# Kernel optimization log

Measured on AMD Instinct MI355X. Metric: run time of the kernel, lower is better.

## Reference

```python
import jax, jax.numpy as jnp
import numpy as np

EPS = 1e-5

def _ln(x, gamma, beta):
    mu = jnp.mean(x, axis=-1, keepdims=True)
    var = jnp.mean(jnp.square(x - mu), axis=-1, keepdims=True)
    return (x - mu) * jax.lax.rsqrt(var + EPS) * gamma + beta

def _linear(x, w, b):
    # torch nn.Linear convention: w is [out, in]
    return jnp.einsum('...i,oi->...o', x, w) + b

def setup_inputs() -> dict:
    key = jax.random.key(0)
    B, L, C = 1, 384, 128
    ks = jax.random.split(key, 16)
    s = 1.0 / np.sqrt(C)
    inp = {
        'pair_feat': jax.random.normal(ks[0], (B, L, L, C), dtype=jnp.float32),
        'res_mask': jnp.ones((B, L), dtype=jnp.float32),
        # left_proj: Linear + LayerNorm
        'lp_w': jax.random.uniform(ks[1], (C, C), jnp.float32, -s, s),
        'lp_b': jnp.zeros((C,), jnp.float32),
        'lp_g': jnp.ones((C,), jnp.float32),
        'lp_beta': jnp.zeros((C,), jnp.float32),
        # right_proj: Linear + LayerNorm
        'rp_w': jax.random.uniform(ks[2], (C, C), jnp.float32, -s, s),
        'rp_b': jnp.zeros((C,), jnp.float32),
        'rp_g': jnp.ones((C,), jnp.float32),
        'rp_beta': jnp.zeros((C,), jnp.float32),
        # gates: Linear (then sigmoid)
        'lg_w': jax.random.uniform(ks[3], (C, C), jnp.float32, -s, s),
        'lg_b': jnp.zeros((C,), jnp.float32),
        'rg_w': jax.random.uniform(ks[4], (C, C), jnp.float32, -s, s),
        'rg_b': jnp.zeros((C,), jnp.float32),
        'og_w': jax.random.uniform(ks[5], (C, C), jnp.float32, -s, s),
        'og_b': jnp.zeros((C,), jnp.float32),
        # out_layer: LayerNorm + Linear
        'ol_g': jnp.ones((C,), jnp.float32),
        'ol_beta': jnp.zeros((C,), jnp.float32),
        'ow': jax.random.uniform(ks[6], (C, C), jnp.float32, -s, s),
        'ob': jnp.zeros((C,), jnp.float32),
    }
    return inp

def reference(pair_feat, res_mask, lp_w, lp_b, lp_g, lp_beta,
              rp_w, rp_b, rp_g, rp_beta, lg_w, lg_b, rg_w, rg_b,
              og_w, og_b, ol_g, ol_beta, ow, ob):
    # op_type == 'outgoing': einsum 'bikc,bjkc->bijc'
    proj_left = _ln(_linear(pair_feat, lp_w, lp_b), lp_g, lp_beta)
    proj_right = _ln(_linear(pair_feat, rp_w, rp_b), rp_g, rp_beta)
    mask2d = (res_mask[:, :, None] * res_mask[:, None, :])[..., None]  # [B,L,L,1]
    proj_left = proj_left * mask2d
    proj_right = proj_right * mask2d
    gate_left = jax.nn.sigmoid(_linear(pair_feat, lg_w, lg_b))
    gate_right = jax.nn.sigmoid(_linear(pair_feat, rg_w, rg_b))
    proj_left = proj_left * gate_left
    proj_right = proj_right * gate_right
    out = jnp.einsum('bikc,bjkc->bijc', proj_left, proj_right)
    out = _linear(_ln(out, ol_g, ol_beta), ow, ob)
    gate = jax.nn.sigmoid(_linear(pair_feat, og_w, og_b))
    return out * gate
```

## Files before the change

### kernel.cpp

```cpp
#include <hip/hip_runtime.h>

typedef __bf16 bf16x8 __attribute__((ext_vector_type(8)));
typedef __bf16 bf16x4 __attribute__((ext_vector_type(4)));
typedef float  f32x4  __attribute__((ext_vector_type(4)));
typedef int    int4v  __attribute__((ext_vector_type(4)));

#define LL    384
#define CC    128
#define NROW  (LL * LL)

#define MFMA16(a, b, c) __builtin_amdgcn_mfma_f32_16x16x32_bf16((a), (b), (c), 0, 0, 0)

__device__ __forceinline__ bf16x8 cvt8(const float* p) {
    f32x4 a = *reinterpret_cast<const f32x4*>(p);
    f32x4 b = *reinterpret_cast<const f32x4*>(p + 4);
    bf16x8 r;
    r[0] = (__bf16)a[0]; r[1] = (__bf16)a[1]; r[2] = (__bf16)a[2]; r[3] = (__bf16)a[3];
    r[4] = (__bf16)b[0]; r[5] = (__bf16)b[1]; r[6] = (__bf16)b[2]; r[7] = (__bf16)b[3];
    return r;
}
__device__ __forceinline__ bf16x8 ld_ws(const __bf16* p) {
    return __builtin_bit_cast(bf16x8, *reinterpret_cast<const int4v*>(p));
}
__device__ __forceinline__ float sigmf(float x) { return 1.f / (1.f + __expf(-x)); }

__device__ __forceinline__ void gl16(const __bf16* g, __bf16* l) {
    __builtin_amdgcn_global_load_lds(
        (const __attribute__((address_space(1))) unsigned int*)g,
        (__attribute__((address_space(3))) unsigned int*)l,
        16, 0, 0);
}

__device__ __forceinline__ void stage_weight(const float* __restrict__ w,
                                             __bf16* dst, int tid) {
    const int c   = tid >> 1;
    const int k0  = (tid & 1) * 64;
    const int nt  = c >> 4;
    const int n16 = c & 15;
    #pragma unroll
    for (int u = 0; u < 8; ++u) {
        const int k    = k0 + u * 8;
        const int ks   = k >> 5;
        const int quad = (k >> 3) & 3;
        bf16x8 v = cvt8(w + c * CC + k);
        *reinterpret_cast<int4v*>(dst + ((ks * 8 + nt) * 64 + quad * 16 + n16) * 8) =
            __builtin_bit_cast(int4v, v);
    }
}
__device__ __forceinline__ bf16x8 wfrag(const __bf16* base, int ks, int nt, int lane) {
    return ld_ws(base + ((ks * 8 + nt) * 64 + lane) * 8);
}

__global__ __launch_bounds__(256) void k_wconv(
    const float* __restrict__ w0, const float* __restrict__ w1,
    const float* __restrict__ w2, const float* __restrict__ w3,
    const float* __restrict__ w4, const float* __restrict__ w5,
    __bf16* __restrict__ dst)
{
    const float* srcs[6] = {w0, w1, w2, w3, w4, w5};
    stage_weight(srcs[blockIdx.x], dst + (size_t)blockIdx.x * 16384, threadIdx.x);
}

__global__ __launch_bounds__(256, 2) void k_proj(
    const float* __restrict__ pf, const float* __restrict__ rmask,
    const __bf16* __restrict__ wfm,
    const float* __restrict__ lp_b, const float* __restrict__ lp_g,
    const float* __restrict__ lp_be,
    const float* __restrict__ rp_b, const float* __restrict__ rp_g,
    const float* __restrict__ rp_be,
    const float* __restrict__ lg_b, const float* __restrict__ rg_b,
    __bf16* __restrict__ pl_c, __bf16* __restrict__ pr_c)
{
    __shared__ __bf16 wl[2][16384];

    const int tid  = threadIdx.x;
    const int wave = tid >> 6, lane = tid & 63;
    const int n16  = lane & 15, quad = lane >> 4;
    const int rowblock = blockIdx.x * 128 + wave * 32;

    auto STAGEW = [&](int widx, __bf16* dstL) {
        const __bf16* src = wfm + (size_t)widx * 16384;
        #pragma unroll
        for (int i = 0; i < 8; ++i) {
            const int s = wave * 8 + i;
            gl16(src + (size_t)s * 512 + lane * 8, dstL + (size_t)s * 512);
        }
    };

    bf16x8 xf[2][4];
    #pragma unroll
    for (int rg = 0; rg < 2; ++rg) {
        const int r_a = rowblock + rg * 16 + n16;
        #pragma unroll
        for (int ks = 0; ks < 4; ++ks)
            xf[rg][ks] = cvt8(pf + (size_t)r_a * CC + ks * 32 + quad * 8);
    }

    float mrow[2][4];
    #pragma unroll
    for (int rg = 0; rg < 2; ++rg) {
        const int rd   = rowblock + rg * 16 + quad * 4;
        const int i_id = rd / LL;
        const int k_id = rd - i_id * LL;
        float mi = rmask[i_id];
        #pragma unroll
        for (int g = 0; g < 4; ++g) mrow[rg][g] = mi * rmask[k_id + g];
    }

    f32x4 acc[2][8];
    auto GEMM = [&](const __bf16* wb) {
        #pragma unroll
        for (int rg = 0; rg < 2; ++rg)
            #pragma unroll
            for (int nt = 0; nt < 8; ++nt) acc[rg][nt] = f32x4{0.f, 0.f, 0.f, 0.f};
        #pragma unroll
        for (int ks = 0; ks < 4; ++ks)
            #pragma unroll
            for (int nt = 0; nt < 8; ++nt) {
                bf16x8 wf = wfrag(wb, ks, nt, lane);
                #pragma unroll
                for (int rg = 0; rg < 2; ++rg)
                    acc[rg][nt] = MFMA16(xf[rg][ks], wf, acc[rg][nt]);
            }
    };

    bf16x4 sg[2][8];
    auto SIGM = [&](const float* gb) {
        #pragma unroll
        for (int rg = 0; rg < 2; ++rg)
            #pragma unroll
            for (int nt = 0; nt < 8; ++nt) {
                float bias = gb[nt * 16 + n16];
                #pragma unroll
                for (int g = 0; g < 4; ++g)
                    sg[rg][nt][g] = (__bf16)sigmf(acc[rg][nt][g] + bias);
            }
    };

    auto EPILOG = [&](const float* pb, const float* gamma, const float* beta,
                      __bf16* dst) {
        #pragma unroll
        for (int rg = 0; rg < 2; ++rg) {
            #pragma unroll
            for (int nt = 0; nt < 8; ++nt) {
                float bias = pb[nt * 16 + n16];
                #pragma unroll
                for (int g = 0; g < 4; ++g) acc[rg][nt][g] += bias;
            }
            float s[4] = {0.f,0.f,0.f,0.f}, ss[4] = {0.f,0.f,0.f,0.f};
            #pragma unroll
            for (int nt = 0; nt < 8; ++nt)
                #pragma unroll
                for (int g = 0; g < 4; ++g) { float v = acc[rg][nt][g]; s[g] += v; ss[g] += v * v; }
            #pragma unroll
            for (int m = 1; m < 16; m <<= 1)
                #pragma unroll
                for (int g = 0; g < 4; ++g) {
                    s[g]  += __shfl_xor(s[g],  m, 64);
                    ss[g] += __shfl_xor(ss[g], m, 64);
                }
            float mean[4], rstd[4];
            #pragma unroll
            for (int g = 0; g < 4; ++g) {
                mean[g] = s[g] * (1.f / 128.f);
                float var = ss[g] * (1.f / 128.f) - mean[g] * mean[g];
                rstd[g] = rsqrtf(fmaxf(var, 0.f) + 1e-5f);
            }
            const int rd = rowblock + rg * 16 + quad * 4;
            #pragma unroll
            for (int nt = 0; nt < 8; ++nt) {
                const int c = nt * 16 + n16;
                float ga = gamma[c], be = beta[c];
                bf16x4 o;
                #pragma unroll
                for (int g = 0; g < 4; ++g) {
                    float v = (acc[rg][nt][g] - mean[g]) * rstd[g] * ga + be;
                    v *= mrow[rg][g] * (float)sg[rg][nt][g];
                    o[g] = (__bf16)v;
                }
                *reinterpret_cast<bf16x4*>(dst + (size_t)c * NROW + rd) = o;
            }
        }
    };

    STAGEW(0, wl[0]);
    __syncthreads();

    STAGEW(1, wl[1]);
    GEMM(wl[0]);  SIGM(lg_b);
    __syncthreads();

    STAGEW(2, wl[0]);
    GEMM(wl[1]);  EPILOG(lp_b, lp_g, lp_be, pl_c);
    __syncthreads();

    STAGEW(3, wl[1]);
    GEMM(wl[0]);  SIGM(rg_b);
    __syncthreads();

    GEMM(wl[1]);  EPILOG(rp_b, rp_g, rp_be, pr_c);
}

__global__ __launch_bounds__(256, 3) void k_einsum_tile(
    const __bf16* __restrict__ pl_c, const __bf16* __restrict__ pr_c,
    float* __restrict__ T)
{
    __shared__ __bf16 sA[2][512 * 8];
    __shared__ __bf16 sB[2][512 * 8];

    const int bid  = blockIdx.x;
    const int wgid = (bid & 7) * 144 + (bid >> 3);
    const int ch   = wgid / 9;
    const int tile = wgid - ch * 9;
    const int i0   = (tile / 3) * 128;
    const int j0   = (tile % 3) * 128;

    const int tid  = threadIdx.x;
    const int w    = tid >> 6, lane = tid & 63;
    const int n16  = lane & 15, quad = lane >> 4;
    const int wr   = w >> 1, wc = w & 1;

    const __bf16* Pc = pl_c + (size_t)ch * NROW;
    const __bf16* Qc = pr_c + (size_t)ch * NROW;

    const __bf16* ga[2];
    const __bf16* gb[2];
    #pragma unroll
    for (int u = 0; u < 2; ++u) {
        const int row = (w * 2 + u) * 16 + n16;
        ga[u] = Pc + (size_t)(i0 + row) * LL + quad * 8;
        gb[u] = Qc + (size_t)(j0 + row) * LL + quad * 8;
    }

    f32x4 acc[4][4];
    #pragma unroll
    for (int m = 0; m < 4; ++m)
        #pragma unroll
        for (int n = 0; n < 4; ++n) acc[m][n] = f32x4{0.f, 0.f, 0.f, 0.f};

    auto STAGE = [&](int buf, int k0) {
        #pragma unroll
        for (int u = 0; u < 2; ++u) {
            __bf16* la = &sA[buf][(size_t)((w * 2 + u) * 64) * 8];
            __bf16* lb = &sB[buf][(size_t)((w * 2 + u) * 64) * 8];
            gl16(ga[u] + k0, la);
            gl16(gb[u] + k0, lb);
        }
    };

    STAGE(0, 0);
    __syncthreads();

    #pragma unroll
    for (int t = 0; t < 12; ++t) {
        if (t < 11) STAGE((t + 1) & 1, (t + 1) * 32);
        const __bf16* Ab = sA[t & 1];
        const __bf16* Bb = sB[t & 1];
        bf16x8 af[4], bf[4];
        #pragma unroll
        for (int m = 0; m < 4; ++m) af[m] = ld_ws(Ab + ((size_t)((wr * 4 + m) * 64 + lane)) * 8);
        #pragma unroll
        for (int n = 0; n < 4; ++n) bf[n] = ld_ws(Bb + ((size_t)((wc * 4 + n) * 64 + lane)) * 8);
        #pragma unroll
        for (int m = 0; m < 4; ++m)
            #pragma unroll
            for (int n = 0; n < 4; ++n)
                acc[m][n] = MFMA16(af[m], bf[n], acc[m][n]);
        __syncthreads();
    }

    float* Tc = T + (size_t)ch * NROW;
    #pragma unroll
    for (int m = 0; m < 4; ++m) {
        const int i = i0 + wr * 64 + m * 16 + quad * 4;
        #pragma unroll
        for (int n = 0; n < 4; ++n) {
            const int j = j0 + wc * 64 + n * 16 + n16;
            #pragma unroll
            for (int g = 0; g < 4; ++g)
                Tc[(size_t)(i + g) * LL + j] = acc[m][n][g];
        }
    }
}

__global__ __launch_bounds__(256, 2) void k_final_cm(
    float* __restrict__ out, const float* __restrict__ T,
    const float* __restrict__ pf, const __bf16* __restrict__ wfm,
    const float* __restrict__ ol_g, const float* __restrict__ ol_be,
    const float* __restrict__ ob,   const float* __restrict__ og_b)
{
    __shared__ __bf16 wl[2][16384];
    const int tid  = threadIdx.x;
    const int wave = tid >> 6, lane = tid & 63;
    const int n16  = lane & 15, quad = lane >> 4;
    const int rowblock = blockIdx.x * 128 + wave * 32;

    #pragma unroll
    for (int i = 0; i < 8; ++i) {
        const int s = wave * 8 + i;
        gl16(wfm + (size_t)(4 * 16384) + (size_t)s * 512 + lane * 8, wl[0] + (size_t)s * 512);
        gl16(wfm + (size_t)(5 * 16384) + (size_t)s * 512 + lane * 8, wl[1] + (size_t)s * 512);
    }
    __syncthreads();

    #pragma unroll
    for (int rg = 0; rg < 2; ++rg) {
        const int r = rowblock + rg * 16 + n16;

        f32x4 tf[8];
        bf16x8 pff[4];
        #pragma unroll
        for (int ks = 0; ks < 4; ++ks) {
            #pragma unroll
            for (int q = 0; q < 4; ++q) {
                tf[2 * ks][q]     = T[(size_t)(ks * 32 + quad * 8 + q)     * NROW + r];
                tf[2 * ks + 1][q] = T[(size_t)(ks * 32 + quad * 8 + 4 + q) * NROW + r];
            }
            pff[ks] = cvt8(pf + (size_t)r * CC + ks * 32 + quad * 8);
        }

        float s = 0.f, ss = 0.f;
        #pragma unroll
        for (int h = 0; h < 8; ++h)
            #pragma unroll
            for (int q = 0; q < 4; ++q) { float f = tf[h][q]; s += f; ss += f * f; }
        s += __shfl_xor(s, 16, 64);  ss += __shfl_xor(ss, 16, 64);
        s += __shfl_xor(s, 32, 64);  ss += __shfl_xor(ss, 32, 64);
        const float mean = s * (1.f / 128.f);
        const float rstd = rsqrtf(fmaxf(ss * (1.f / 128.f) - mean * mean, 0.f) + 1e-5f);

        bf16x8 xn[4];
        #pragma unroll
        for (int ks = 0; ks < 4; ++ks) {
            const int cb = ks * 32 + quad * 8;
            f32x4 g0 = *reinterpret_cast<const f32x4*>(ol_g + cb);
            f32x4 g1 = *reinterpret_cast<const f32x4*>(ol_g + cb + 4);
            f32x4 b0 = *reinterpret_cast<const f32x4*>(ol_be + cb);
            f32x4 b1 = *reinterpret_cast<const f32x4*>(ol_be + cb + 4);
            bf16x8 rv;
            #pragma unroll
            for (int q = 0; q < 4; ++q) {
                rv[q]     = (__bf16)((tf[2 * ks][q]     - mean) * rstd * g0[q] + b0[q]);
                rv[4 + q] = (__bf16)((tf[2 * ks + 1][q] - mean) * rstd * g1[q] + b1[q]);
            }
            xn[ks] = rv;
        }

        f32x4 ao[8], ag[8];
        #pragma unroll
        for (int mt = 0; mt < 8; ++mt) { ao[mt] = f32x4{0.f,0.f,0.f,0.f}; ag[mt] = f32x4{0.f,0.f,0.f,0.f}; }
        #pragma unroll
        for (int ks = 0; ks < 4; ++ks)
            #pragma unroll
            for (int mt = 0; mt < 8; ++mt) {
                bf16x8 awf = wfrag(wl[0], ks, mt, lane);
                bf16x8 gwf = wfrag(wl[1], ks, mt, lane);
                ao[mt] = MFMA16(awf, xn[ks],  ao[mt]);
                ag[mt] = MFMA16(gwf, pff[ks], ag[mt]);
            }

        #pragma unroll
        for (int mt = 0; mt < 8; ++mt) {
            const int c0 = mt * 16 + quad * 4;
            f32x4 bb = *reinterpret_cast<const f32x4*>(ob + c0);
            f32x4 gb = *reinterpret_cast<const f32x4*>(og_b + c0);
            f32x4 o;
            #pragma unroll
            for (int g = 0; g < 4; ++g) {
                float gate = sigmf(ag[mt][g] + gb[g]);
                o[g] = (ao[mt][g] + bb[g]) * gate;
            }
            *reinterpret_cast<f32x4*>(out + (size_t)r * CC + c0) = o;
        }
    }
}

__global__ __launch_bounds__(256, 2) void k_proj_fb(
    const float* __restrict__ pf, const float* __restrict__ rmask,
    const float* __restrict__ lp_w, const float* __restrict__ lp_b,
    const float* __restrict__ lp_g, const float* __restrict__ lp_be,
    const float* __restrict__ rp_w, const float* __restrict__ rp_b,
    const float* __restrict__ rp_g, const float* __restrict__ rp_be,
    const float* __restrict__ lg_w, const float* __restrict__ lg_b,
    const float* __restrict__ rg_w, const float* __restrict__ rg_b,
    __bf16* __restrict__ pl_c, __bf16* __restrict__ pr_c)
{
    __shared__ __bf16 wl[2 * 16384];

    const int tid  = threadIdx.x;
    const int wave = tid >> 6, lane = tid & 63;
    const int n16  = lane & 15, quad = lane >> 4;
    const int rowblock = blockIdx.x * 128 + wave * 32;

    bf16x8 xf[2][4];
    #pragma unroll
    for (int rg = 0; rg < 2; ++rg) {
        const int r_a = rowblock + rg * 16 + n16;
        #pragma unroll
        for (int ks = 0; ks < 4; ++ks)
            xf[rg][ks] = cvt8(pf + (size_t)r_a * CC + ks * 32 + quad * 8);
    }

    float mrow[2][4];
    #pragma unroll
    for (int rg = 0; rg < 2; ++rg) {
        const int rd   = rowblock + rg * 16 + quad * 4;
        const int i_id = rd / LL;
        const int k_id = rd - i_id * LL;
        float mi = rmask[i_id];
        #pragma unroll
        for (int g = 0; g < 4; ++g) mrow[rg][g] = mi * rmask[k_id + g];
    }

    auto phase = [&](const float* gw, const float* gb,
                     const float* pw, const float* pb,
                     const float* gamma, const float* beta,
                     __bf16* dst) {
        stage_weight(gw, wl, tid);
        stage_weight(pw, wl + 16384, tid);
        __syncthreads();

        f32x4 acc[2][8];
        #pragma unroll
        for (int rg = 0; rg < 2; ++rg)
            #pragma unroll
            for (int nt = 0; nt < 8; ++nt) acc[rg][nt] = f32x4{0.f, 0.f, 0.f, 0.f};
        #pragma unroll
        for (int ks = 0; ks < 4; ++ks)
            #pragma unroll
            for (int nt = 0; nt < 8; ++nt) {
                bf16x8 wf = wfrag(wl, ks, nt, lane);
                #pragma unroll
                for (int rg = 0; rg < 2; ++rg)
                    acc[rg][nt] = MFMA16(xf[rg][ks], wf, acc[rg][nt]);
            }
        bf16x4 sg[2][8];
        #pragma unroll
        for (int rg = 0; rg < 2; ++rg)
            #pragma unroll
            for (int nt = 0; nt < 8; ++nt) {
                float bias = gb[nt * 16 + n16];
                #pragma unroll
                for (int g = 0; g < 4; ++g)
                    sg[rg][nt][g] = (__bf16)sigmf(acc[rg][nt][g] + bias);
            }
        #pragma unroll
        for (int rg = 0; rg < 2; ++rg)
            #pragma unroll
            for (int nt = 0; nt < 8; ++nt) acc[rg][nt] = f32x4{0.f, 0.f, 0.f, 0.f};
        #pragma unroll
        for (int ks = 0; ks < 4; ++ks)
            #pragma unroll
            for (int nt = 0; nt < 8; ++nt) {
                bf16x8 wf = wfrag(wl + 16384, ks, nt, lane);
                #pragma unroll
                for (int rg = 0; rg < 2; ++rg)
                    acc[rg][nt] = MFMA16(xf[rg][ks], wf, acc[rg][nt]);
            }
        #pragma unroll
        for (int rg = 0; rg < 2; ++rg) {
            #pragma unroll
            for (int nt = 0; nt < 8; ++nt) {
                float bias = pb[nt * 16 + n16];
                #pragma unroll
                for (int g = 0; g < 4; ++g) acc[rg][nt][g] += bias;
            }
            float s[4] = {0.f,0.f,0.f,0.f}, ss[4] = {0.f,0.f,0.f,0.f};
            #pragma unroll
            for (int nt = 0; nt < 8; ++nt)
                #pragma unroll
                for (int g = 0; g < 4; ++g) { float v = acc[rg][nt][g]; s[g] += v; ss[g] += v * v; }
            #pragma unroll
            for (int m = 1; m < 16; m <<= 1)
                #pragma unroll
                for (int g = 0; g < 4; ++g) {
                    s[g]  += __shfl_xor(s[g],  m, 64);
                    ss[g] += __shfl_xor(ss[g], m, 64);
                }
            float mean[4], rstd[4];
            #pragma unroll
            for (int g = 0; g < 4; ++g) {
                mean[g] = s[g] * (1.f / 128.f);
                float var = ss[g] * (1.f / 128.f) - mean[g] * mean[g];
                rstd[g] = rsqrtf(fmaxf(var, 0.f) + 1e-5f);
            }
            const int rd = rowblock + rg * 16 + quad * 4;
            #pragma unroll
            for (int nt = 0; nt < 8; ++nt) {
                const int c = nt * 16 + n16;
                float ga = gamma[c], be = beta[c];
                bf16x4 o;
                #pragma unroll
                for (int g = 0; g < 4; ++g) {
                    float v = (acc[rg][nt][g] - mean[g]) * rstd[g] * ga + be;
                    v *= mrow[rg][g] * (float)sg[rg][nt][g];
                    o[g] = (__bf16)v;
                }
                *reinterpret_cast<bf16x4*>(dst + (size_t)c * NROW + rd) = o;
            }
        }
        __syncthreads();
    };

    phase(lg_w, lg_b, lp_w, lp_b, lp_g, lp_be, pl_c);
    phase(rg_w, rg_b, rp_w, rp_b, rp_g, rp_be, pr_c);
}

__global__ __launch_bounds__(256, 2) void k_einsum_direct(
    const __bf16* __restrict__ pl_c, const __bf16* __restrict__ pr_c,
    float* __restrict__ out)
{
    const int tid  = threadIdx.x;
    const int wave = tid >> 6, lane = tid & 63;
    const int n16  = lane & 15, quad = lane >> 4;
    const int i0   = blockIdx.x * 64;
    const int jw   = blockIdx.y * 64 + wave * 16;
    const int c0   = blockIdx.z * 8;

    size_t off_i[4];
    #pragma unroll
    for (int t = 0; t < 4; ++t)
        off_i[t] = (size_t)(i0 + t * 16 + n16) * LL + quad * 8;
    const size_t off_j = (size_t)(jw + n16) * LL + quad * 8;

    f32x4 acc[8][4];
    #pragma unroll
    for (int c = 0; c < 8; ++c)
        #pragma unroll
        for (int t = 0; t < 4; ++t) acc[c][t] = f32x4{0.f, 0.f, 0.f, 0.f};

    #pragma unroll
    for (int c = 0; c < 8; ++c) {
        const __bf16* Pb = pl_c + (size_t)(c0 + c) * NROW;
        const __bf16* Qb = pr_c + (size_t)(c0 + c) * NROW + off_j;
        #pragma unroll
        for (int kt = 0; kt < 12; ++kt) {
            bf16x8 fj = ld_ws(Qb + kt * 32);
            #pragma unroll
            for (int t = 0; t < 4; ++t) {
                bf16x8 fi = ld_ws(Pb + off_i[t] + kt * 32);
                acc[c][t] = MFMA16(fi, fj, acc[c][t]);
            }
        }
    }

    #pragma unroll
    for (int t = 0; t < 4; ++t)
        #pragma unroll
        for (int g = 0; g < 4; ++g) {
            const int i = i0 + t * 16 + quad * 4 + g;
            float* dst = out + ((size_t)i * LL + jw + n16) * CC + c0;
            f32x4 lo, hi;
            #pragma unroll
            for (int q = 0; q < 4; ++q) { lo[q] = acc[q][t][g]; hi[q] = acc[4 + q][t][g]; }
            *reinterpret_cast<f32x4*>(dst)     = lo;
            *reinterpret_cast<f32x4*>(dst + 4) = hi;
        }
}

__global__ __launch_bounds__(256, 2) void k_final_ip(
    float* out, const float* __restrict__ pf,
    const float* __restrict__ ol_g, const float* __restrict__ ol_be,
    const float* __restrict__ ow,   const float* __restrict__ ob,
    const float* __restrict__ og_w, const float* __restrict__ og_b)
{
    __shared__ __bf16 wl[2 * 16384];
    const int tid  = threadIdx.x;
    const int wave = tid >> 6, lane = tid & 63;
    const int n16  = lane & 15, quad = lane >> 4;
    const int rowblock = blockIdx.x * 128 + wave * 32;

    stage_weight(ow,   wl,         tid);
    stage_weight(og_w, wl + 16384, tid);
    __syncthreads();

    #pragma unroll
    for (int rg = 0; rg < 2; ++rg) {
        const int r = rowblock + rg * 16 + n16;

        f32x4 tf[8];
        bf16x8 pff[4];
        #pragma unroll
        for (int ks = 0; ks < 4; ++ks) {
            const float* tp = out + (size_t)r * CC + ks * 32 + quad * 8;
            tf[2 * ks]     = *reinterpret_cast<const f32x4*>(tp);
            tf[2 * ks + 1] = *reinterpret_cast<const f32x4*>(tp + 4);
            pff[ks] = cvt8(pf + (size_t)r * CC + ks * 32 + quad * 8);
        }

        float s = 0.f, ss = 0.f;
        #pragma unroll
        for (int h = 0; h < 8; ++h)
            #pragma unroll
            for (int q = 0; q < 4; ++q) { float f = tf[h][q]; s += f; ss += f * f; }
        s += __shfl_xor(s, 16, 64);  ss += __shfl_xor(ss, 16, 64);
        s += __shfl_xor(s, 32, 64);  ss += __shfl_xor(ss, 32, 64);
        const float mean = s * (1.f / 128.f);
        const float rstd = rsqrtf(fmaxf(ss * (1.f / 128.f) - mean * mean, 0.f) + 1e-5f);

        bf16x8 xn[4];
        #pragma unroll
        for (int ks = 0; ks < 4; ++ks) {
            const int cb = ks * 32 + quad * 8;
            f32x4 g0 = *reinterpret_cast<const f32x4*>(ol_g + cb);
            f32x4 g1 = *reinterpret_cast<const f32x4*>(ol_g + cb + 4);
            f32x4 b0 = *reinterpret_cast<const f32x4*>(ol_be + cb);
            f32x4 b1 = *reinterpret_cast<const f32x4*>(ol_be + cb + 4);
            bf16x8 rv;
            #pragma unroll
            for (int q = 0; q < 4; ++q) {
                rv[q]     = (__bf16)((tf[2 * ks][q]     - mean) * rstd * g0[q] + b0[q]);
                rv[4 + q] = (__bf16)((tf[2 * ks + 1][q] - mean) * rstd * g1[q] + b1[q]);
            }
            xn[ks] = rv;
        }

        f32x4 ao[8], ag[8];
        #pragma unroll
        for (int mt = 0; mt < 8; ++mt) { ao[mt] = f32x4{0.f,0.f,0.f,0.f}; ag[mt] = f32x4{0.f,0.f,0.f,0.f}; }
        #pragma unroll
        for (int ks = 0; ks < 4; ++ks)
            #pragma unroll
            for (int mt = 0; mt < 8; ++mt) {
                bf16x8 awf = wfrag(wl,         ks, mt, lane);
                bf16x8 gwf = wfrag(wl + 16384, ks, mt, lane);
                ao[mt] = MFMA16(awf, xn[ks],  ao[mt]);
                ag[mt] = MFMA16(gwf, pff[ks], ag[mt]);
            }

        #pragma unroll
        for (int mt = 0; mt < 8; ++mt) {
            const int c0 = mt * 16 + quad * 4;
            f32x4 bb = *reinterpret_cast<const f32x4*>(ob + c0);
            f32x4 gb = *reinterpret_cast<const f32x4*>(og_b + c0);
            f32x4 o;
            #pragma unroll
            for (int g = 0; g < 4; ++g) {
                float gate = sigmf(ag[mt][g] + gb[g]);
                o[g] = (ao[mt][g] + bb[g]) * gate;
            }
            *reinterpret_cast<f32x4*>(out + (size_t)r * CC + c0) = o;
        }
    }
}

extern "C" void kernel_launch(void* const* d_in, const int* in_sizes, int n_in,
                              void* d_out, int out_size, void* d_ws, size_t ws_size,
                              hipStream_t stream)
{
    const float* pf    = (const float*)d_in[0];
    const float* rmask = (const float*)d_in[1];
    const float* lp_w  = (const float*)d_in[2];
    const float* lp_b  = (const float*)d_in[3];
    const float* lp_g  = (const float*)d_in[4];
    const float* lp_be = (const float*)d_in[5];
    const float* rp_w  = (const float*)d_in[6];
    const float* rp_b  = (const float*)d_in[7];
    const float* rp_g  = (const float*)d_in[8];
    const float* rp_be = (const float*)d_in[9];
    const float* lg_w  = (const float*)d_in[10];
    const float* lg_b  = (const float*)d_in[11];
    const float* rg_w  = (const float*)d_in[12];
    const float* rg_b  = (const float*)d_in[13];
    const float* og_w  = (const float*)d_in[14];
    const float* og_b  = (const float*)d_in[15];
    const float* ol_g  = (const float*)d_in[16];
    const float* ol_be = (const float*)d_in[17];
    const float* ow    = (const float*)d_in[18];
    const float* ob    = (const float*)d_in[19];
    float* out = (float*)d_out;

    __bf16* pl_c = (__bf16*)d_ws;
    __bf16* pr_c = pl_c + (size_t)CC * NROW;
    __bf16* wfm  = pr_c + (size_t)CC * NROW;
    float*  T    = (float*)(wfm + 6 * 16384);

    const size_t need = (size_t)CC * NROW * (2 + 2 + 4) + 6 * 16384 * 2;

    if (ws_size >= need) {
        k_wconv<<<6, 256, 0, stream>>>(lg_w, lp_w, rg_w, rp_w, ow, og_w, wfm);
        k_proj<<<NROW / 128, 256, 0, stream>>>(pf, rmask, wfm,
            lp_b, lp_g, lp_be, rp_b, rp_g, rp_be, lg_b, rg_b, pl_c, pr_c);
        k_einsum_tile<<<1152, 256, 0, stream>>>(pl_c, pr_c, T);
        k_final_cm<<<NROW / 128, 256, 0, stream>>>(out, T, pf, wfm,
            ol_g, ol_be, ob, og_b);
    } else {
        k_proj_fb<<<NROW / 128, 256, 0, stream>>>(pf, rmask,
            lp_w, lp_b, lp_g, lp_be, rp_w, rp_b, rp_g, rp_be,
            lg_w, lg_b, rg_w, rg_b, pl_c, pr_c);
        k_einsum_direct<<<dim3(LL / 64, LL / 64, CC / 8), 256, 0, stream>>>(pl_c, pr_c, out);
        k_final_ip<<<NROW / 128, 256, 0, stream>>>(out, pf,
            ol_g, ol_be, ow, ob, og_w, og_b);
    }
}
```

Before: 312.7 us.

## Single-buffer projection weights in LDS to raise k_proj occupancy to three blocks

Replaces the double-buffered 64KB weight staging in LDS with one 32KB buffer and raises the k_proj launch-bounds occupancy hint from 2 to 3 blocks per CU. The next weight load now starts after the current GEMM finishes and overlaps only the sigmoid/epilogue work, with extra barriers around the shared buffer. The aim is to hide latency with more resident blocks, at the cost of less load/compute overlap inside each block and tighter register limits.

```diff
diff --git a/kernel.cpp b/kernel.cpp
--- a/kernel.cpp
+++ b/kernel.cpp
@@ -61,7 +61,7 @@
     stage_weight(srcs[blockIdx.x], dst + (size_t)blockIdx.x * 16384, threadIdx.x);
 }
 
-__global__ __launch_bounds__(256, 2) void k_proj(
+__global__ __launch_bounds__(256, 3) void k_proj(
     const float* __restrict__ pf, const float* __restrict__ rmask,
     const __bf16* __restrict__ wfm,
     const float* __restrict__ lp_b, const float* __restrict__ lp_g,
@@ -71,19 +71,19 @@
     const float* __restrict__ lg_b, const float* __restrict__ rg_b,
     __bf16* __restrict__ pl_c, __bf16* __restrict__ pr_c)
 {
-    __shared__ __bf16 wl[2][16384];
+    __shared__ __bf16 wl[16384];
 
     const int tid  = threadIdx.x;
     const int wave = tid >> 6, lane = tid & 63;
     const int n16  = lane & 15, quad = lane >> 4;
     const int rowblock = blockIdx.x * 128 + wave * 32;
 
-    auto STAGEW = [&](int widx, __bf16* dstL) {
+    auto STAGEW = [&](int widx) {
         const __bf16* src = wfm + (size_t)widx * 16384;
         #pragma unroll
         for (int i = 0; i < 8; ++i) {
             const int s = wave * 8 + i;
-            gl16(src + (size_t)s * 512 + lane * 8, dstL + (size_t)s * 512);
+            gl16(src + (size_t)s * 512 + lane * 8, wl + (size_t)s * 512);
         }
     };
 
@@ -108,7 +108,7 @@
     }
 
     f32x4 acc[2][8];
-    auto GEMM = [&](const __bf16* wb) {
+    auto GEMM = [&]() {
         #pragma unroll
         for (int rg = 0; rg < 2; ++rg)
             #pragma unroll
@@ -117,7 +117,7 @@
         for (int ks = 0; ks < 4; ++ks)
             #pragma unroll
             for (int nt = 0; nt < 8; ++nt) {
-                bf16x8 wf = wfrag(wb, ks, nt, lane);
+                bf16x8 wf = wfrag(wl, ks, nt, lane);
                 #pragma unroll
                 for (int rg = 0; rg < 2; ++rg)
                     acc[rg][nt] = MFMA16(xf[rg][ks], wf, acc[rg][nt]);
@@ -183,22 +183,29 @@
         }
     };
 
-    STAGEW(0, wl[0]);
-    __syncthreads();
-
-    STAGEW(1, wl[1]);
-    GEMM(wl[0]);  SIGM(lg_b);
-    __syncthreads();
-
-    STAGEW(2, wl[0]);
-    GEMM(wl[1]);  EPILOG(lp_b, lp_g, lp_be, pl_c);
-    __syncthreads();
-
-    STAGEW(3, wl[1]);
-    GEMM(wl[0]);  SIGM(rg_b);
-    __syncthreads();
-
-    GEMM(wl[1]);  EPILOG(rp_b, rp_g, rp_be, pr_c);
+    STAGEW(0);
+    __syncthreads();
+
+    GEMM();
+    __syncthreads();
+    STAGEW(1);
+    SIGM(lg_b);
+    __syncthreads();
+
+    GEMM();
+    __syncthreads();
+    STAGEW(2);
+    EPILOG(lp_b, lp_g, lp_be, pl_c);
+    __syncthreads();
+
+    GEMM();
+    __syncthreads();
+    STAGEW(3);
+    SIGM(rg_b);
+    __syncthreads();
+
+    GEMM();
+    EPILOG(rp_b, rp_g, rp_be, pr_c);
 }
 
 __global__ __launch_bounds__(256, 3) void k_einsum_tile(
```

After: 386.5 us. 23.6% more time.
